# Kernel optimization log

Hardware: AMD Instinct MI355X
Metric: run time of the kernel (lower is better)

## Reference

```python
import jax, jax.numpy as jnp
import numpy as np

C = 768
H = 12
HD = C // H
SCALE = HD ** -0.5
EPS = 1e-5


def setup_inputs() -> dict:
    key = jax.random.key(0)
    kit = iter(jax.random.split(key, 40))
    r = lambda *s: jax.random.normal(next(kit), s, jnp.float32) * 0.02
    d = dict(
        s_x=jax.random.normal(next(kit), (8, 196, C), jnp.float32),
        t_x=jax.random.normal(next(kit), (8, 1568, C), jnp.float32),
        ln1s_g=jnp.ones(C), ln1s_b=jnp.zeros(C),
        mha_w=r(3 * C, C), mha_b=r(3 * C), mha_ow=r(C, C), mha_ob=r(C),
        ln1t_g=jnp.ones(C), ln1t_b=jnp.zeros(C),
        attn_qkv_w=r(3 * C, C), attn_q_b=r(C), attn_v_b=r(C), attn_pw=r(C, C), attn_pb=r(C),
        lnt2s_g=jnp.ones(C), lnt2s_b=jnp.zeros(C),
        t2s_qw=r(C, C), t2s_qb=r(C), t2s_kvw=r(2 * C, C), t2s_kvb=r(C), t2s_pw=r(C, C), t2s_pb=r(C),
        lns2t_g=jnp.ones(C), lns2t_b=jnp.zeros(C),
        s2t_qw=r(C, C), s2t_qb=r(C), s2t_kvw=r(2 * C, C), s2t_kvb=r(C), s2t_pw=r(C, C), s2t_pb=r(C),
        ln2s_g=jnp.ones(C), ln2s_b=jnp.zeros(C),
        cfc_w=r(4 * C, C), cfc_b=r(4 * C), cproj_w=r(C, 4 * C), cproj_b=r(C),
        ln2t_g=jnp.ones(C), ln2t_b=jnp.zeros(C),
        fc1_w=r(4 * C, C), fc1_b=r(4 * C), fc2_w=r(C, 4 * C), fc2_b=r(C),
    )
    return d


def ln(x, g, b):
    m = x.mean(-1, keepdims=True)
    v = jnp.mean((x - m) ** 2, -1, keepdims=True)
    return (x - m) * jax.lax.rsqrt(v + EPS) * g + b


def heads(x):  # (B, N, C) -> (B, H, N, HD)
    B, N, _ = x.shape
    return x.reshape(B, N, H, HD).transpose(0, 2, 1, 3)


def mhsa(q, k, v):  # (B, H, Nq, HD), (B, H, Nk, HD) -> (B, Nq, C)
    a = jax.nn.softmax(jnp.einsum('bhqd,bhkd->bhqk', q * SCALE, k), axis=-1)
    o = jnp.einsum('bhqk,bhkd->bhqd', a, v)
    B, _, Nq, _ = o.shape
    return o.transpose(0, 2, 1, 3).reshape(B, Nq, C)


def reference(s_x, t_x, ln1s_g, ln1s_b, mha_w, mha_b, mha_ow, mha_ob,
              ln1t_g, ln1t_b, attn_qkv_w, attn_q_b, attn_v_b, attn_pw, attn_pb,
              lnt2s_g, lnt2s_b, t2s_qw, t2s_qb, t2s_kvw, t2s_kvb, t2s_pw, t2s_pb,
              lns2t_g, lns2t_b, s2t_qw, s2t_qb, s2t_kvw, s2t_kvb, s2t_pw, s2t_pb,
              ln2s_g, ln2s_b, cfc_w, cfc_b, cproj_w, cproj_b,
              ln2t_g, ln2t_b, fc1_w, fc1_b, fc2_w, fc2_b):
    # 1) clip self-attention. torch nn.MultiheadAttention (batch_first=False)
    # treats axis 0 of the (B, s_N, C) input as the sequence dim, so we
    # faithfully attend over the batch axis.
    y = ln(s_x, ln1s_g, ln1s_b)
    qkv = y @ mha_w.T + mha_b  # (B, s_N, 3C)
    q, k, v = jnp.split(qkv, 3, axis=-1)
    qt, kt, vt = (a.transpose(1, 0, 2) for a in (q, k, v))  # (s_N, B, C)
    o = mhsa(heads(qt), heads(kt), heads(vt))  # (s_N, B, C)
    o = o @ mha_ow.T + mha_ob
    s_x = s_x + o.transpose(1, 0, 2)

    # 2) video-stream self-attention (qkv_bias=True -> cat(q_b, 0, v_b))
    y = ln(t_x, ln1t_g, ln1t_b)
    qkv_bias = jnp.concatenate([attn_q_b, jnp.zeros_like(attn_v_b), attn_v_b])
    qkv = y @ attn_qkv_w.T + qkv_bias
    q, k, v = jnp.split(qkv, 3, axis=-1)
    o = mhsa(heads(q), heads(k), heads(v))
    t_x = t_x + (o @ attn_pw.T + attn_pb)

    # 3) T2S cross: query from LN(s_x), key/value from (updated, un-normed) t_x
    ys = ln(s_x, lnt2s_g, lnt2s_b)
    q = ys @ t2s_qw.T + t2s_qb
    kv = t_x @ t2s_kvw.T + jnp.concatenate([jnp.zeros_like(t2s_kvb), t2s_kvb])
    k, v = jnp.split(kv, 2, axis=-1)
    o = mhsa(heads(q), heads(k), heads(v))
    s_x = s_x + (o @ t2s_pw.T + t2s_pb)

    # 4) S2T cross: query from LN(t_x), key/value from updated s_x
    yt = ln(t_x, lns2t_g, lns2t_b)
    q = yt @ s2t_qw.T + s2t_qb
    kv = s_x @ s2t_kvw.T + jnp.concatenate([jnp.zeros_like(s2t_kvb), s2t_kvb])
    k, v = jnp.split(kv, 2, axis=-1)
    o = mhsa(heads(q), heads(k), heads(v))
    t_x = t_x + (o @ s2t_pw.T + s2t_pb)

    # 5) clip MLP (QuickGELU)
    y = ln(s_x, ln2s_g, ln2s_b)
    h = y @ cfc_w.T + cfc_b
    h = h * jax.nn.sigmoid(1.702 * h)
    s_x = s_x + (h @ cproj_w.T + cproj_b)

    # 6) video MLP (exact GELU, torch default)
    y = ln(t_x, ln2t_g, ln2t_b)
    h = jax.nn.gelu(y @ fc1_w.T + fc1_b, approximate=False)
    t_x = t_x + (h @ fc2_w.T + fc2_b)
    return (s_x, t_x)
```

## Files before the change

### kernel.cpp

```cpp
#include <hip/hip_runtime.h>
#include <stdint.h>


typedef uint16_t u16;
typedef uint16_t u16x8 __attribute__((ext_vector_type(8)));
typedef uint16_t u16x4 __attribute__((ext_vector_type(4)));
typedef short bf16x8 __attribute__((ext_vector_type(8)));
typedef float f32x4 __attribute__((ext_vector_type(4)));

__device__ __forceinline__ float b2f(u16 u) {
    union { float f; uint32_t i; } x;
    x.i = ((uint32_t)u) << 16;
    return x.f;
}
__device__ __forceinline__ u16 f2b(float f) {
    union { float f; uint32_t i; } x;
    x.f = f;
    uint32_t i = x.i;
    uint32_t r = (i + 0x7FFFu + ((i >> 16) & 1u)) >> 16;
    return (u16)r;
}
__device__ __forceinline__ u16 f2b_trunc(float f) {
    union { float f; uint32_t i; } x;
    x.f = f;
    return (u16)(x.i >> 16);
}

__device__ __forceinline__ void gload16(const u16* g, u16* l) {
    __builtin_amdgcn_global_load_lds(
        (const __attribute__((address_space(1))) uint32_t*)g,
        (__attribute__((address_space(3))) uint32_t*)l, 16, 0, 0);
}

__global__ void f2b_kernel(const float* __restrict__ in, u16* __restrict__ out, int n) {
    int i = blockIdx.x * 256 + threadIdx.x;
    if (i < n) out[i] = f2b(in[i]);
}
__global__ void copy_f32(const float* __restrict__ in, float* __restrict__ out, int n) {
    int i = blockIdx.x * 256 + threadIdx.x;
    if (i < n) out[i] = in[i];
}

__global__ void build_bias_pool(float* __restrict__ dst,
    const float* mha_b, const float* attn_q_b, const float* attn_v_b,
    const float* mha_ob, const float* attn_pb, const float* t2s_kvb,
    const float* t2s_qb, const float* t2s_pb, const float* s2t_qb,
    const float* s2t_kvb, const float* s2t_pb, const float* cfc_b,
    const float* cproj_b, const float* fc1_b, const float* fc2_b) {
    int i = blockIdx.x * 256 + threadIdx.x;
    float v = 0.f;
    if (i < 2304) v = mha_b[i];
    else if (i < 4608) { int j = i - 2304; v = (j < 768) ? attn_q_b[j] : (j < 1536 ? 0.f : attn_v_b[j - 1536]); }
    else if (i < 5376) v = mha_ob[i - 4608];
    else if (i < 6144) v = attn_pb[i - 5376];
    else if (i < 7680) { int j = i - 6144; v = (j < 768) ? 0.f : t2s_kvb[j - 768]; }
    else if (i < 8448) v = t2s_qb[i - 7680];
    else if (i < 9216) v = t2s_pb[i - 8448];
    else if (i < 9984) v = s2t_qb[i - 9216];
    else if (i < 11520) { int j = i - 9984; v = (j < 768) ? 0.f : s2t_kvb[j - 768]; }
    else if (i < 12288) v = s2t_pb[i - 11520];
    else if (i < 15360) v = cfc_b[i - 12288];
    else if (i < 16128) v = cproj_b[i - 15360];
    else if (i < 19200) v = fc1_b[i - 16128];
    else if (i < 19968) v = fc2_b[i - 19200];
    else return;
    dst[i] = v;
}

__device__ __forceinline__ float block_sum(float v, float* red) {
    #pragma unroll
    for (int o = 32; o > 0; o >>= 1) v += __shfl_down(v, o, 64);
    int w = threadIdx.x >> 6, l = threadIdx.x & 63;
    __syncthreads();
    if (l == 0) red[w] = v;
    __syncthreads();
    return red[0] + red[1] + red[2] + red[3];
}

__global__ __launch_bounds__(256) void ln_kernel(
    const float* __restrict__ x, const float* __restrict__ g,
    const float* __restrict__ bta, u16* __restrict__ y) {
    const int r = blockIdx.x;
    const int t = threadIdx.x;
    const float* xr = x + (size_t)r * 768;
    float v0 = xr[t], v1 = xr[t + 256], v2 = xr[t + 512];
    __shared__ float red[4];
    float mean = block_sum(v0 + v1 + v2, red) * (1.0f / 768.0f);
    float d0 = v0 - mean, d1 = v1 - mean, d2 = v2 - mean;
    float var = block_sum(d0 * d0 + d1 * d1 + d2 * d2, red) * (1.0f / 768.0f);
    float rs = rsqrtf(var + 1e-5f);
    u16* yr = y + (size_t)r * 768;
    yr[t]       = f2b(d0 * rs * g[t]       + bta[t]);
    yr[t + 256] = f2b(d1 * rs * g[t + 256] + bta[t + 256]);
    yr[t + 512] = f2b(d2 * rs * g[t + 512] + bta[t + 512]);
}

__global__ __launch_bounds__(256) void transpose_v(
    const u16* __restrict__ vp, u16* __restrict__ vt, int Nk, int Nkp,
    long long vA, long long vJ) {
    const int inst = blockIdx.y;
    const int a = inst / 12, h = inst % 12;
    const int t0 = blockIdx.x * 64;
    const int tid = threadIdx.x;
    __shared__ u16 T[64][72];
    const int kvl = tid >> 2, dseg = (tid & 3) * 16;
    u16x8 v0 = {}, v1 = {};
    if (t0 + kvl < Nk) {
        const u16* src = vp + a * vA + (long long)(t0 + kvl) * vJ + h * 64 + dseg;
        v0 = *(const u16x8*)src;
        v1 = *(const u16x8*)(src + 8);
    }
    *(u16x8*)&T[kvl][dseg]     = v0;
    *(u16x8*)&T[kvl][dseg + 8] = v1;
    __syncthreads();
    const int dl = tid >> 2, kseg = (tid & 3) * 16;
    u16x8 w0, w1;
    #pragma unroll
    for (int j = 0; j < 8; j++) w0[j] = T[kseg + j][dl];
    #pragma unroll
    for (int j = 0; j < 8; j++) w1[j] = T[kseg + 8 + j][dl];
    u16* orow = vt + ((size_t)inst * 64 + dl) * Nkp + t0 + kseg;
    *(u16x8*)orow = w0;
    *(u16x8*)(orow + 8) = w1;
}

template <int MODE, int BM>
__global__ __launch_bounds__(256) void gemm_mfma(
    const u16* __restrict__ A, const u16* __restrict__ W,
    const float* __restrict__ bias, u16* __restrict__ Cb,
    float* __restrict__ Cf, int M, int N, int K) {
    constexpr int MI = BM / 32;
    __shared__ u16 As[2][BM][32];
    __shared__ u16 Bs[2][128][32];
    const int tid = threadIdx.x;
    const int lane = tid & 63;
    const int wid = tid >> 6;
    const int wr = (wid >> 1) * (BM / 2), wc = (wid & 1) * 64;
    const int m0 = blockIdx.x * BM, n0 = blockIdx.y * 128;
    const int lr = lane >> 2, lc = (lane & 3) * 8;
    const int fr = lane & 15, fk = (lane >> 4) * 8;
    const int abase = wid * (BM / 4);
    const int bbase = wid * 32;
    f32x4 acc[MI][4] = {};
    for (int k0 = 0; k0 < K; k0 += 64) {
        #pragma unroll
        for (int s = 0; s < 2; s++) {
            #pragma unroll
            for (int j = 0; j < BM / 64; j++) {
                int rowa = m0 + abase + j * 16 + lr;
                rowa = rowa < M ? rowa : M - 1;
                gload16(A + (size_t)rowa * K + k0 + s * 32 + lc, &As[s][abase + j * 16][0]);
            }
            #pragma unroll
            for (int j = 0; j < 2; j++) {
                gload16(W + (size_t)(n0 + bbase + j * 16 + lr) * K + k0 + s * 32 + lc,
                        &Bs[s][bbase + j * 16][0]);
            }
        }
        __syncthreads();
        #pragma unroll
        for (int s = 0; s < 2; s++) {
            bf16x8 a[MI], b[4];
            #pragma unroll
            for (int i = 0; i < MI; i++) a[i] = *(const bf16x8*)&As[s][wr + i * 16 + fr][fk];
            #pragma unroll
            for (int j = 0; j < 4; j++) b[j] = *(const bf16x8*)&Bs[s][wc + j * 16 + fr][fk];
            #pragma unroll
            for (int i = 0; i < MI; i++)
                #pragma unroll
                for (int j = 0; j < 4; j++)
                    acc[i][j] = __builtin_amdgcn_mfma_f32_16x16x32_bf16(a[i], b[j], acc[i][j], 0, 0, 0);
        }
        __syncthreads();
    }
    const int er = (lane >> 4) * 4;
    #pragma unroll
    for (int i = 0; i < MI; i++) {
        #pragma unroll
        for (int reg = 0; reg < 4; reg++) {
            int r = m0 + wr + i * 16 + er + reg;
            if (r >= M) continue;
            #pragma unroll
            for (int j = 0; j < 4; j++) {
                int c = n0 + wc + j * 16 + fr;
                float v = acc[i][j][reg] + bias[c];
                size_t idx = (size_t)r * N + c;
                if (MODE == 1) {
                    Cf[idx] += v;
                } else if (MODE == 4) {
                    float nv = Cf[idx] + v;
                    Cf[idx] = nv;
                    Cb[idx] = f2b(nv);
                } else {
                    if (MODE == 2) v = v / (1.0f + expf(-1.702f * v));
                    if (MODE == 3) v = 0.5f * v * (1.0f + erff(v * 0.70710678118654752f));
                    Cb[idx] = f2b(v);
                }
            }
        }
    }
}

__global__ __launch_bounds__(256) void flash_attn(
    const u16* __restrict__ qp, const u16* __restrict__ kp,
    const u16* __restrict__ vt, u16* __restrict__ op,
    int Nq, int Nk, int Nkp,
    long long qA, long long qI, long long kA, long long kJ,
    long long oA, long long oI) {
    const int inst = blockIdx.y;
    const int a = inst / 12, h = inst % 12;
    const int tid = threadIdx.x, lane = tid & 63, w = tid >> 6;
    const int fr = lane & 15, g = lane >> 4, fk = g * 8;
    const int f3s = (fr & 7) << 3;
    __shared__ u16 Ks[2][64][64];
    __shared__ u16 Vs[2][64][64];
    __shared__ u16 Ps[4][16][64];
    const u16* qb = qp + a * qA + h * 64;
    const u16* kb = kp + a * kA + h * 64;
    const u16* vtb = vt + (size_t)inst * 64 * Nkp;
    const int q0 = blockIdx.x * 64 + w * 16;

    bf16x8 qf[2];
    {
        u16x8 raw0 = {}, raw1 = {};
        int qr = q0 + fr;
        if (qr < Nq) {
            const u16* qrp = qb + (long long)qr * qI;
            raw0 = *(const u16x8*)(qrp + fk);
            raw1 = *(const u16x8*)(qrp + 32 + fk);
        }
        const float QS = 0.125f * 1.44269504088896340736f;
        u16x8 s0, s1;
        #pragma unroll
        for (int e = 0; e < 8; e++) {
            s0[e] = f2b(b2f(raw0[e]) * QS);
            s1[e] = f2b(b2f(raw1[e]) * QS);
        }
        qf[0] = *(bf16x8*)&s0;
        qf[1] = *(bf16x8*)&s1;
    }
    float mrun = -1e30f, lrun = 0.f;
    f32x4 o[4] = {};

    const int l = lane;
    const int srow = w * 8 + (l >> 3);
    const int sdcol = ((l & 7) * 8) ^ (((l >> 3) & 7) << 3);

    auto STAGE = [&](int s, int t0) {
        #pragma unroll
        for (int c = 0; c < 2; c++) {
            int row = c * 32 + srow;
            int kr = t0 + row; if (kr >= Nk) kr = Nk - 1;
            gload16(kb + (long long)kr * kJ + sdcol, &Ks[s][0][0] + c * 2048 + w * 512);
            gload16(vtb + (size_t)row * Nkp + t0 + sdcol, &Vs[s][0][0] + c * 2048 + w * 512);
        }
    };

    const int nt = (Nk + 63) >> 6;
    STAGE(0, 0);
    for (int it = 0; it < nt; ++it) {
        const int t0 = it << 6;
        const int cur = it & 1;
        if (it + 1 < nt) {
            STAGE(cur ^ 1, t0 + 64);
            asm volatile("s_waitcnt vmcnt(4)" ::: "memory");
        } else {
            asm volatile("s_waitcnt vmcnt(0)" ::: "memory");
        }
        __builtin_amdgcn_s_barrier();

        f32x4 s[4] = {};
        __builtin_amdgcn_s_setprio(1);
        #pragma unroll
        for (int hh = 0; hh < 4; hh++) {
            bf16x8 k0f = *(const bf16x8*)&Ks[cur][hh * 16 + fr][fk ^ f3s];
            bf16x8 k1f = *(const bf16x8*)&Ks[cur][hh * 16 + fr][(32 + fk) ^ f3s];
            s[hh] = __builtin_amdgcn_mfma_f32_16x16x32_bf16(k0f, qf[0], s[hh], 0, 0, 0);
            s[hh] = __builtin_amdgcn_mfma_f32_16x16x32_bf16(k1f, qf[1], s[hh], 0, 0, 0);
        }
        __builtin_amdgcn_s_setprio(0);

        if (t0 + 64 > Nk) {
            #pragma unroll
            for (int hh = 0; hh < 4; hh++)
                #pragma unroll
                for (int r = 0; r < 4; r++)
                    if (t0 + hh * 16 + 4 * g + r >= Nk) s[hh][r] = -1e30f;
        }
        float a0 = fmaxf(fmaxf(s[0][0], s[0][1]), s[0][2]);
        float a1 = fmaxf(fmaxf(s[0][3], s[1][0]), s[1][1]);
        float a2 = fmaxf(fmaxf(s[1][2], s[1][3]), s[2][0]);
        float a3 = fmaxf(fmaxf(s[2][1], s[2][2]), s[2][3]);
        float a4 = fmaxf(fmaxf(s[3][0], s[3][1]), s[3][2]);
        float b0 = fmaxf(fmaxf(a0, a1), a2);
        float b1 = fmaxf(fmaxf(a3, a4), s[3][3]);
        float lmax = fmaxf(b0, b1);
        lmax = fmaxf(lmax, __shfl_xor(lmax, 16, 64));
        lmax = fmaxf(lmax, __shfl_xor(lmax, 32, 64));
        if (!__all(lmax <= mrun + 8.0f)) {
            float mn = fmaxf(mrun, lmax);
            float sf = exp2f(mrun - mn);
            mrun = mn;
            lrun *= sf;
            float sfo[4];
            #pragma unroll
            for (int r = 0; r < 4; r++) sfo[r] = __shfl(sf, g * 4 + r, 64);
            #pragma unroll
            for (int dt = 0; dt < 4; dt++)
                #pragma unroll
                for (int r = 0; r < 4; r++) o[dt][r] *= sfo[r];
        }
        float p[4][4];
        float ps = 0.f;
        #pragma unroll
        for (int hh = 0; hh < 4; hh++)
            #pragma unroll
            for (int r = 0; r < 4; r++) {
                p[hh][r] = exp2f(s[hh][r] - mrun);
                ps += p[hh][r];
            }
        ps += __shfl_xor(ps, 16, 64);
        ps += __shfl_xor(ps, 32, 64);
        lrun += ps;
        #pragma unroll
        for (int hh = 0; hh < 4; hh++) {
            u16x4 pk;
            #pragma unroll
            for (int r = 0; r < 4; r++) pk[r] = f2b_trunc(p[hh][r]);
            *(u16x4*)&Ps[w][fr][(hh * 16 + g * 4) ^ f3s] = pk;
        }
        bf16x8 pa0 = *(const bf16x8*)&Ps[w][fr][fk ^ f3s];
        bf16x8 pa1 = *(const bf16x8*)&Ps[w][fr][(32 + fk) ^ f3s];
        __builtin_amdgcn_s_setprio(1);
        #pragma unroll
        for (int dt = 0; dt < 4; dt++) {
            bf16x8 vf0 = *(const bf16x8*)&Vs[cur][dt * 16 + fr][fk ^ f3s];
            bf16x8 vf1 = *(const bf16x8*)&Vs[cur][dt * 16 + fr][(32 + fk) ^ f3s];
            o[dt] = __builtin_amdgcn_mfma_f32_16x16x32_bf16(pa0, vf0, o[dt], 0, 0, 0);
            o[dt] = __builtin_amdgcn_mfma_f32_16x16x32_bf16(pa1, vf1, o[dt], 0, 0, 0);
        }
        __builtin_amdgcn_s_setprio(0);
        __builtin_amdgcn_s_barrier();
    }
    float rcp = 1.0f / lrun;
    #pragma unroll
    for (int r = 0; r < 4; r++) {
        float rr = __shfl(rcp, g * 4 + r, 64);
        int q = q0 + g * 4 + r;
        if (q >= Nq) continue;
        u16* orow = op + a * oA + (long long)q * oI + h * 64;
        #pragma unroll
        for (int dt = 0; dt < 4; dt++)
            orow[dt * 16 + fr] = f2b(o[dt][r] * rr);
    }
}

extern "C" void kernel_launch(void* const* d_in, const int* in_sizes, int n_in,
                              void* d_out, int out_size, void* d_ws, size_t ws_size,
                              hipStream_t stream) {
    const int B = 8, sN = 196, tN = 1568;
    const int Ms = B * sN;
    const int Mt = B * tN;
    const int n_sf = Ms * 768;
    const int n_tf = Mt * 768;
    (void)n_in; (void)out_size; (void)ws_size;

    const bool dict_order = (in_sizes[0] == n_sf);
    auto IN = [&](int di, int ai) -> const float* {
        return (const float*)d_in[dict_order ? di : ai];
    };
    const float* in_sx      = IN(0, 35);
    const float* in_tx      = IN(1, 42);
    const float* ln1s_g     = IN(2, 14);
    const float* ln1s_b     = IN(3, 13);
    const float* mha_w      = IN(4, 28);
    const float* mha_b      = IN(5, 25);
    const float* mha_ow     = IN(6, 27);
    const float* mha_ob     = IN(7, 26);
    const float* ln1t_g     = IN(8, 16);
    const float* ln1t_b     = IN(9, 15);
    const float* attn_qkv_w = IN(10, 3);
    const float* attn_q_b   = IN(11, 2);
    const float* attn_v_b   = IN(12, 4);
    const float* attn_pw    = IN(13, 1);
    const float* attn_pb    = IN(14, 0);
    const float* lnt2s_g    = IN(15, 24);
    const float* lnt2s_b    = IN(16, 23);
    const float* t2s_qw     = IN(17, 41);
    const float* t2s_qb     = IN(18, 40);
    const float* t2s_kvw    = IN(19, 37);
    const float* t2s_kvb    = IN(20, 36);
    const float* t2s_pw     = IN(21, 39);
    const float* t2s_pb     = IN(22, 38);
    const float* lns2t_g    = IN(23, 22);
    const float* lns2t_b    = IN(24, 21);
    const float* s2t_qw     = IN(25, 34);
    const float* s2t_qb     = IN(26, 33);
    const float* s2t_kvw    = IN(27, 30);
    const float* s2t_kvb    = IN(28, 29);
    const float* s2t_pw     = IN(29, 32);
    const float* s2t_pb     = IN(30, 31);
    const float* ln2s_g     = IN(31, 18);
    const float* ln2s_b     = IN(32, 17);
    const float* cfc_w      = IN(33, 6);
    const float* cfc_b      = IN(34, 5);
    const float* cproj_w    = IN(35, 8);
    const float* cproj_b    = IN(36, 7);
    const float* ln2t_g     = IN(37, 20);
    const float* ln2t_b     = IN(38, 19);
    const float* fc1_w      = IN(39, 10);
    const float* fc1_b      = IN(40, 9);
    const float* fc2_w      = IN(41, 12);
    const float* fc2_b      = IN(42, 11);

    float* s_f = (float*)d_out;
    float* t_f = (float*)d_out + n_sf;

    char* ws = (char*)d_ws;
    size_t off = 0;
    auto take = [&](size_t bytes) { size_t o = off; off += (bytes + 255) & ~(size_t)255; return o; };
    float* biasP = (float*)(ws + take(19968 * 4));
    u16*   yb    = (u16*)(ws + take((size_t)Mt * 768 * 2));
    u16*   bufA  = (u16*)(ws + take((size_t)Mt * 3072 * 2));
    u16*   bufB  = (u16*)(ws + take((size_t)Mt * 768 * 2));
    u16*   sxb   = (u16*)(ws + take((size_t)Ms * 768 * 2));
    u16*   vtb   = (u16*)(ws + take((size_t)2352 * 64 * 64 * 2));
    auto wtake = [&](size_t nelem) { return (u16*)(ws + take(nelem * 2)); };
    u16 *W_mha   = wtake(2304 * 768), *W_mhao  = wtake(768 * 768);
    u16 *W_qkv   = wtake(2304 * 768), *W_attnp = wtake(768 * 768);
    u16 *W_t2sq  = wtake(768 * 768),  *W_t2skv = wtake(1536 * 768), *W_t2sp = wtake(768 * 768);
    u16 *W_s2tq  = wtake(768 * 768),  *W_s2tkv = wtake(1536 * 768), *W_s2tp = wtake(768 * 768);
    u16 *W_cfc   = wtake(3072 * 768), *W_cproj = wtake(768 * 3072);
    u16 *W_fc1   = wtake(3072 * 768), *W_fc2   = wtake(768 * 3072);

    const int B_MHA = 0, B_QKV = 2304, B_MHAO = 4608, B_ATTNP = 5376;
    const int B_T2SKV = 6144, B_T2SQ = 7680, B_T2SP = 8448, B_S2TQ = 9216;
    const int B_S2TKV = 9984, B_S2TP = 11520, B_CFC = 12288, B_CPROJ = 15360;
    const int B_FC1 = 16128, B_FC2 = 19200;

    auto cdiv = [](int a, int b) { return (a + b - 1) / b; };
    auto CW = [&](const float* src, u16* dst, int n) {
        f2b_kernel<<<cdiv(n, 256), 256, 0, stream>>>(src, dst, n);
    };
    CW(mha_w, W_mha, 2304 * 768);      CW(mha_ow, W_mhao, 768 * 768);
    CW(attn_qkv_w, W_qkv, 2304 * 768); CW(attn_pw, W_attnp, 768 * 768);
    CW(t2s_qw, W_t2sq, 768 * 768);     CW(t2s_kvw, W_t2skv, 1536 * 768);
    CW(t2s_pw, W_t2sp, 768 * 768);     CW(s2t_qw, W_s2tq, 768 * 768);
    CW(s2t_kvw, W_s2tkv, 1536 * 768);  CW(s2t_pw, W_s2tp, 768 * 768);
    CW(cfc_w, W_cfc, 3072 * 768);      CW(cproj_w, W_cproj, 768 * 3072);
    CW(fc1_w, W_fc1, 3072 * 768);      CW(fc2_w, W_fc2, 768 * 3072);

    build_bias_pool<<<78, 256, 0, stream>>>(biasP,
        mha_b, attn_q_b, attn_v_b, mha_ob, attn_pb, t2s_kvb, t2s_qb, t2s_pb,
        s2t_qb, s2t_kvb, s2t_pb, cfc_b, cproj_b, fc1_b, fc2_b);

    copy_f32<<<cdiv(n_sf, 256), 256, 0, stream>>>(in_sx, s_f, n_sf);
    copy_f32<<<cdiv(n_tf, 256), 256, 0, stream>>>(in_tx, t_f, n_tf);

    ln_kernel<<<Ms, 256, 0, stream>>>(s_f, ln1s_g, ln1s_b, yb);
    gemm_mfma<0, 64><<<dim3(cdiv(Ms, 64), 18), 256, 0, stream>>>(yb, W_mha, biasP + B_MHA, bufA, (float*)0, Ms, 2304, 768);
    transpose_v<<<dim3(1, sN * 12), 256, 0, stream>>>(bufA + 1536, vtb, 8, 64, 2304LL, (long long)sN * 2304);
    flash_attn<<<dim3(1, sN * 12), 256, 0, stream>>>(
        bufA, bufA + 768, vtb, bufB, 8, 8, 64,
        2304LL, (long long)sN * 2304,
        2304LL, (long long)sN * 2304,
        768LL,  (long long)sN * 768);
    gemm_mfma<1, 64><<<dim3(cdiv(Ms, 64), 6), 256, 0, stream>>>(bufB, W_mhao, biasP + B_MHAO, (u16*)0, s_f, Ms, 768, 768);

    ln_kernel<<<Mt, 256, 0, stream>>>(t_f, ln1t_g, ln1t_b, yb);
    gemm_mfma<0, 128><<<dim3(cdiv(Mt, 128), 18), 256, 0, stream>>>(yb, W_qkv, biasP + B_QKV, bufA, (float*)0, Mt, 2304, 768);
    transpose_v<<<dim3(25, B * 12), 256, 0, stream>>>(bufA + 1536, vtb, tN, 1600, (long long)tN * 2304, 2304LL);
    flash_attn<<<dim3(cdiv(tN, 64), B * 12), 256, 0, stream>>>(
        bufA, bufA + 768, vtb, bufB, tN, tN, 1600,
        (long long)tN * 2304, 2304LL,
        (long long)tN * 2304, 2304LL,
        (long long)tN * 768, 768LL);
    gemm_mfma<4, 128><<<dim3(cdiv(Mt, 128), 6), 256, 0, stream>>>(bufB, W_attnp, biasP + B_ATTNP, yb, t_f, Mt, 768, 768);

    gemm_mfma<0, 128><<<dim3(cdiv(Mt, 128), 12), 256, 0, stream>>>(yb, W_t2skv, biasP + B_T2SKV, bufA, (float*)0, Mt, 1536, 768);
    transpose_v<<<dim3(25, B * 12), 256, 0, stream>>>(bufA + 768, vtb, tN, 1600, (long long)tN * 1536, 1536LL);
    ln_kernel<<<Ms, 256, 0, stream>>>(s_f, lnt2s_g, lnt2s_b, yb);
    u16* q3 = bufB;
    u16* o3 = bufB + (size_t)Ms * 768;
    gemm_mfma<0, 64><<<dim3(cdiv(Ms, 64), 6), 256, 0, stream>>>(yb, W_t2sq, biasP + B_T2SQ, q3, (float*)0, Ms, 768, 768);
    flash_attn<<<dim3(cdiv(sN, 64), B * 12), 256, 0, stream>>>(
        q3, bufA, vtb, o3, sN, tN, 1600,
        (long long)sN * 768, 768LL,
        (long long)tN * 1536, 1536LL,
        (long long)sN * 768, 768LL);
    gemm_mfma<4, 64><<<dim3(cdiv(Ms, 64), 6), 256, 0, stream>>>(o3, W_t2sp, biasP + B_T2SP, sxb, s_f, Ms, 768, 768);

    ln_kernel<<<Mt, 256, 0, stream>>>(t_f, lns2t_g, lns2t_b, yb);
    gemm_mfma<0, 128><<<dim3(cdiv(Mt, 128), 6), 256, 0, stream>>>(yb, W_s2tq, biasP + B_S2TQ, bufB, (float*)0, Mt, 768, 768);
    gemm_mfma<0, 64><<<dim3(cdiv(Ms, 64), 12), 256, 0, stream>>>(sxb, W_s2tkv, biasP + B_S2TKV, bufA, (float*)0, Ms, 1536, 768);
    transpose_v<<<dim3(4, B * 12), 256, 0, stream>>>(bufA + 768, vtb, sN, 256, (long long)sN * 1536, 1536LL);
    flash_attn<<<dim3(cdiv(tN, 64), B * 12), 256, 0, stream>>>(
        bufB, bufA, vtb, yb, tN, sN, 256,
        (long long)tN * 768, 768LL,
        (long long)sN * 1536, 1536LL,
        (long long)tN * 768, 768LL);
    gemm_mfma<1, 128><<<dim3(cdiv(Mt, 128), 6), 256, 0, stream>>>(yb, W_s2tp, biasP + B_S2TP, (u16*)0, t_f, Mt, 768, 768);

    ln_kernel<<<Ms, 256, 0, stream>>>(s_f, ln2s_g, ln2s_b, yb);
    gemm_mfma<2, 64><<<dim3(cdiv(Ms, 64), 24), 256, 0, stream>>>(yb, W_cfc, biasP + B_CFC, bufA, (float*)0, Ms, 3072, 768);
    gemm_mfma<1, 64><<<dim3(cdiv(Ms, 64), 6), 256, 0, stream>>>(bufA, W_cproj, biasP + B_CPROJ, (u16*)0, s_f, Ms, 768, 3072);

    ln_kernel<<<Mt, 256, 0, stream>>>(t_f, ln2t_g, ln2t_b, yb);
    gemm_mfma<3, 128><<<dim3(cdiv(Mt, 128), 24), 256, 0, stream>>>(yb, W_fc1, biasP + B_FC1, bufA, (float*)0, Mt, 3072, 768);
    gemm_mfma<1, 128><<<dim3(cdiv(Mt, 128), 6), 256, 0, stream>>>(bufA, W_fc2, biasP + B_FC2, (u16*)0, t_f, Mt, 768, 3072);
}
```

Before: 1.050 ms.

## Co-launch independent spatial and temporal stream kernels as paired grids

Adds paired kernel wrappers for the GEMM, flash-attention, transpose and layernorm kernels. One launch now runs both the small spatial-stream problem and the large temporal-stream problem, chosen by flattened block index. The fourteen weight conversions collapse into one segmented kernel and the two input copies into one. This is meant to fill the GPU better on the small s-stream kernels and to cut launch count. In exchange it adds new buffer aliasing (vtb_s shares yb), relies on s_f and t_f being contiguous in the output, and gives each paired kernel shared-memory sizing for the larger tile.

```diff
diff --git a/kernel.cpp b/kernel.cpp
--- a/kernel.cpp
+++ b/kernel.cpp
@@ -32,16 +32,29 @@
         (__attribute__((address_space(3))) uint32_t*)l, 16, 0, 0);
 }
 
-__global__ void f2b_kernel(const float* __restrict__ in, u16* __restrict__ out, int n) {
+struct CvtAll {
+    const float* s[14];
+    u16* d[14];
+    int cum[15];
+};
+__global__ __launch_bounds__(256) void cvt_all(CvtAll c) {
     int i = blockIdx.x * 256 + threadIdx.x;
-    if (i < n) out[i] = f2b(in[i]);
-}
-__global__ void copy_f32(const float* __restrict__ in, float* __restrict__ out, int n) {
+    if (i >= c.cum[14]) return;
+    int seg = 0;
+    #pragma unroll
+    for (int k = 1; k < 14; k++) seg += (i >= c.cum[k]);
+    int j = i - c.cum[seg];
+    c.d[seg][j] = f2b(c.s[seg][j]);
+}
+
+__global__ __launch_bounds__(256) void copy_both(
+    const float* __restrict__ a, const float* __restrict__ b,
+    float* __restrict__ out, int na, int ntot) {
     int i = blockIdx.x * 256 + threadIdx.x;
-    if (i < n) out[i] = in[i];
-}
-
-__global__ void build_bias_pool(float* __restrict__ dst,
+    if (i < ntot) out[i] = (i < na) ? a[i] : b[i - na];
+}
+
+__global__ __launch_bounds__(256) void build_bias_pool(float* __restrict__ dst,
     const float* mha_b, const float* attn_q_b, const float* attn_v_b,
     const float* mha_ob, const float* attn_pb, const float* t2s_kvb,
     const float* t2s_qb, const float* t2s_pb, const float* s2t_qb,
@@ -77,11 +90,15 @@
     return red[0] + red[1] + red[2] + red[3];
 }
 
-__global__ __launch_bounds__(256) void ln_kernel(
-    const float* __restrict__ x, const float* __restrict__ g,
-    const float* __restrict__ bta, u16* __restrict__ y) {
+__global__ __launch_bounds__(256) void ln_dual(
+    const float* __restrict__ x, int rows0,
+    const float* __restrict__ g0, const float* __restrict__ b0, u16* __restrict__ y0,
+    const float* __restrict__ g1, const float* __restrict__ b1, u16* __restrict__ y1) {
     const int r = blockIdx.x;
     const int t = threadIdx.x;
+    const float* g; const float* bta; u16* yr;
+    if (r < rows0) { g = g0; bta = b0; yr = y0 + (size_t)r * 768; }
+    else           { g = g1; bta = b1; yr = y1 + (size_t)(r - rows0) * 768; }
     const float* xr = x + (size_t)r * 768;
     float v0 = xr[t], v1 = xr[t + 256], v2 = xr[t + 512];
     __shared__ float red[4];
@@ -89,24 +106,25 @@
     float d0 = v0 - mean, d1 = v1 - mean, d2 = v2 - mean;
     float var = block_sum(d0 * d0 + d1 * d1 + d2 * d2, red) * (1.0f / 768.0f);
     float rs = rsqrtf(var + 1e-5f);
-    u16* yr = y + (size_t)r * 768;
     yr[t]       = f2b(d0 * rs * g[t]       + bta[t]);
     yr[t + 256] = f2b(d1 * rs * g[t + 256] + bta[t + 256]);
     yr[t + 512] = f2b(d2 * rs * g[t + 512] + bta[t + 512]);
 }
 
-__global__ __launch_bounds__(256) void transpose_v(
-    const u16* __restrict__ vp, u16* __restrict__ vt, int Nk, int Nkp,
-    long long vA, long long vJ) {
-    const int inst = blockIdx.y;
+struct TransP {
+    const u16* vp; u16* vt;
+    int Nk, Nkp, gx, nb;
+    long long vA, vJ;
+};
+__device__ __forceinline__ void transpose_body(const TransP p, int bid, u16 (*T)[72]) {
+    const int x = bid % p.gx, inst = bid / p.gx;
     const int a = inst / 12, h = inst % 12;
-    const int t0 = blockIdx.x * 64;
+    const int t0 = x * 64;
     const int tid = threadIdx.x;
-    __shared__ u16 T[64][72];
     const int kvl = tid >> 2, dseg = (tid & 3) * 16;
     u16x8 v0 = {}, v1 = {};
-    if (t0 + kvl < Nk) {
-        const u16* src = vp + a * vA + (long long)(t0 + kvl) * vJ + h * 64 + dseg;
+    if (t0 + kvl < p.Nk) {
+        const u16* src = p.vp + a * p.vA + (long long)(t0 + kvl) * p.vJ + h * 64 + dseg;
         v0 = *(const u16x8*)src;
         v1 = *(const u16x8*)(src + 8);
     }
@@ -119,42 +137,51 @@
     for (int j = 0; j < 8; j++) w0[j] = T[kseg + j][dl];
     #pragma unroll
     for (int j = 0; j < 8; j++) w1[j] = T[kseg + 8 + j][dl];
-    u16* orow = vt + ((size_t)inst * 64 + dl) * Nkp + t0 + kseg;
+    u16* orow = p.vt + ((size_t)inst * 64 + dl) * p.Nkp + t0 + kseg;
     *(u16x8*)orow = w0;
     *(u16x8*)(orow + 8) = w1;
 }
-
+__global__ __launch_bounds__(256) void transpose_pair(TransP p0, TransP p1) {
+    __shared__ u16 T[64][72];
+    int bid = blockIdx.x;
+    if (bid < p0.nb) transpose_body(p0, bid, T);
+    else transpose_body(p1, bid - p0.nb, T);
+}
+
+struct GemmP {
+    const u16* A; const u16* W; const float* bias;
+    u16* Cb; float* Cf;
+    int M, N, K, gx, nb;
+};
 template <int MODE, int BM>
-__global__ __launch_bounds__(256) void gemm_mfma(
-    const u16* __restrict__ A, const u16* __restrict__ W,
-    const float* __restrict__ bias, u16* __restrict__ Cb,
-    float* __restrict__ Cf, int M, int N, int K) {
+__device__ __forceinline__ void gemm_body(const GemmP p, int bid,
+                                          u16 (*AsF)[32], u16 (*BsF)[32]) {
     constexpr int MI = BM / 32;
-    __shared__ u16 As[2][BM][32];
-    __shared__ u16 Bs[2][128][32];
     const int tid = threadIdx.x;
     const int lane = tid & 63;
     const int wid = tid >> 6;
     const int wr = (wid >> 1) * (BM / 2), wc = (wid & 1) * 64;
-    const int m0 = blockIdx.x * BM, n0 = blockIdx.y * 128;
+    const int bx = bid % p.gx, by = bid / p.gx;
+    const int m0 = bx * BM, n0 = by * 128;
     const int lr = lane >> 2, lc = (lane & 3) * 8;
     const int fr = lane & 15, fk = (lane >> 4) * 8;
     const int abase = wid * (BM / 4);
     const int bbase = wid * 32;
     f32x4 acc[MI][4] = {};
-    for (int k0 = 0; k0 < K; k0 += 64) {
+    for (int k0 = 0; k0 < p.K; k0 += 64) {
         #pragma unroll
         for (int s = 0; s < 2; s++) {
             #pragma unroll
             for (int j = 0; j < BM / 64; j++) {
                 int rowa = m0 + abase + j * 16 + lr;
-                rowa = rowa < M ? rowa : M - 1;
-                gload16(A + (size_t)rowa * K + k0 + s * 32 + lc, &As[s][abase + j * 16][0]);
+                rowa = rowa < p.M ? rowa : p.M - 1;
+                gload16(p.A + (size_t)rowa * p.K + k0 + s * 32 + lc,
+                        &AsF[s * 128 + abase + j * 16][0]);
             }
             #pragma unroll
             for (int j = 0; j < 2; j++) {
-                gload16(W + (size_t)(n0 + bbase + j * 16 + lr) * K + k0 + s * 32 + lc,
-                        &Bs[s][bbase + j * 16][0]);
+                gload16(p.W + (size_t)(n0 + bbase + j * 16 + lr) * p.K + k0 + s * 32 + lc,
+                        &BsF[s * 128 + bbase + j * 16][0]);
             }
         }
         __syncthreads();
@@ -162,9 +189,9 @@
         for (int s = 0; s < 2; s++) {
             bf16x8 a[MI], b[4];
             #pragma unroll
-            for (int i = 0; i < MI; i++) a[i] = *(const bf16x8*)&As[s][wr + i * 16 + fr][fk];
-            #pragma unroll
-            for (int j = 0; j < 4; j++) b[j] = *(const bf16x8*)&Bs[s][wc + j * 16 + fr][fk];
+            for (int i = 0; i < MI; i++) a[i] = *(const bf16x8*)&AsF[s * 128 + wr + i * 16 + fr][fk];
+            #pragma unroll
+            for (int j = 0; j < 4; j++) b[j] = *(const bf16x8*)&BsF[s * 128 + wc + j * 16 + fr][fk];
             #pragma unroll
             for (int i = 0; i < MI; i++)
                 #pragma unroll
@@ -179,53 +206,59 @@
         #pragma unroll
         for (int reg = 0; reg < 4; reg++) {
             int r = m0 + wr + i * 16 + er + reg;
-            if (r >= M) continue;
+            if (r >= p.M) continue;
             #pragma unroll
             for (int j = 0; j < 4; j++) {
                 int c = n0 + wc + j * 16 + fr;
-                float v = acc[i][j][reg] + bias[c];
-                size_t idx = (size_t)r * N + c;
+                float v = acc[i][j][reg] + p.bias[c];
+                size_t idx = (size_t)r * p.N + c;
                 if (MODE == 1) {
-                    Cf[idx] += v;
+                    p.Cf[idx] += v;
                 } else if (MODE == 4) {
-                    float nv = Cf[idx] + v;
-                    Cf[idx] = nv;
-                    Cb[idx] = f2b(nv);
+                    float nv = p.Cf[idx] + v;
+                    p.Cf[idx] = nv;
+                    p.Cb[idx] = f2b(nv);
                 } else {
                     if (MODE == 2) v = v / (1.0f + expf(-1.702f * v));
                     if (MODE == 3) v = 0.5f * v * (1.0f + erff(v * 0.70710678118654752f));
-                    Cb[idx] = f2b(v);
+                    p.Cb[idx] = f2b(v);
                 }
             }
         }
     }
 }
-
-__global__ __launch_bounds__(256) void flash_attn(
-    const u16* __restrict__ qp, const u16* __restrict__ kp,
-    const u16* __restrict__ vt, u16* __restrict__ op,
-    int Nq, int Nk, int Nkp,
-    long long qA, long long qI, long long kA, long long kJ,
-    long long oA, long long oI) {
-    const int inst = blockIdx.y;
+template <int M0, int B0, int M1, int B1>
+__global__ __launch_bounds__(256) void gemm_pair(GemmP p0, GemmP p1) {
+    __shared__ u16 As[2 * 128][32];
+    __shared__ u16 Bs[2 * 128][32];
+    int bid = blockIdx.x;
+    if (bid < p0.nb) gemm_body<M0, B0>(p0, bid, As, Bs);
+    else gemm_body<M1, B1>(p1, bid - p0.nb, As, Bs);
+}
+
+struct FlashP {
+    const u16* qp; const u16* kp; const u16* vt; u16* op;
+    int Nq, Nk, Nkp, gx, nb;
+    long long qA, qI, kA, kJ, oA, oI;
+};
+__device__ __forceinline__ void flash_body(const FlashP p, int bid,
+    u16 (*Ks)[64][64], u16 (*Vs)[64][64], u16 (*Ps)[16][64]) {
+    const int x = bid % p.gx, inst = bid / p.gx;
     const int a = inst / 12, h = inst % 12;
     const int tid = threadIdx.x, lane = tid & 63, w = tid >> 6;
     const int fr = lane & 15, g = lane >> 4, fk = g * 8;
     const int f3s = (fr & 7) << 3;
-    __shared__ u16 Ks[2][64][64];
-    __shared__ u16 Vs[2][64][64];
-    __shared__ u16 Ps[4][16][64];
-    const u16* qb = qp + a * qA + h * 64;
-    const u16* kb = kp + a * kA + h * 64;
-    const u16* vtb = vt + (size_t)inst * 64 * Nkp;
-    const int q0 = blockIdx.x * 64 + w * 16;
+    const u16* qb = p.qp + a * p.qA + h * 64;
+    const u16* kb = p.kp + a * p.kA + h * 64;
+    const u16* vtb = p.vt + (size_t)inst * 64 * p.Nkp;
+    const int q0 = x * 64 + w * 16;
 
     bf16x8 qf[2];
     {
         u16x8 raw0 = {}, raw1 = {};
         int qr = q0 + fr;
-        if (qr < Nq) {
-            const u16* qrp = qb + (long long)qr * qI;
+        if (qr < p.Nq) {
+            const u16* qrp = qb + (long long)qr * p.qI;
             raw0 = *(const u16x8*)(qrp + fk);
             raw1 = *(const u16x8*)(qrp + 32 + fk);
         }
@@ -250,13 +283,13 @@
         #pragma unroll
         for (int c = 0; c < 2; c++) {
             int row = c * 32 + srow;
-            int kr = t0 + row; if (kr >= Nk) kr = Nk - 1;
-            gload16(kb + (long long)kr * kJ + sdcol, &Ks[s][0][0] + c * 2048 + w * 512);
-            gload16(vtb + (size_t)row * Nkp + t0 + sdcol, &Vs[s][0][0] + c * 2048 + w * 512);
+            int kr = t0 + row; if (kr >= p.Nk) kr = p.Nk - 1;
+            gload16(kb + (long long)kr * p.kJ + sdcol, &Ks[s][0][0] + c * 2048 + w * 512);
+            gload16(vtb + (size_t)row * p.Nkp + t0 + sdcol, &Vs[s][0][0] + c * 2048 + w * 512);
         }
     };
 
-    const int nt = (Nk + 63) >> 6;
+    const int nt = (p.Nk + 63) >> 6;
     STAGE(0, 0);
     for (int it = 0; it < nt; ++it) {
         const int t0 = it << 6;
@@ -280,12 +313,12 @@
         }
         __builtin_amdgcn_s_setprio(0);
 
-        if (t0 + 64 > Nk) {
+        if (t0 + 64 > p.Nk) {
             #pragma unroll
             for (int hh = 0; hh < 4; hh++)
                 #pragma unroll
                 for (int r = 0; r < 4; r++)
-                    if (t0 + hh * 16 + 4 * g + r >= Nk) s[hh][r] = -1e30f;
+                    if (t0 + hh * 16 + 4 * g + r >= p.Nk) s[hh][r] = -1e30f;
         }
         float a0 = fmaxf(fmaxf(s[0][0], s[0][1]), s[0][2]);
         float a1 = fmaxf(fmaxf(s[0][3], s[1][0]), s[1][1]);
@@ -310,14 +343,14 @@
                 #pragma unroll
                 for (int r = 0; r < 4; r++) o[dt][r] *= sfo[r];
         }
-        float p[4][4];
+        float pp[4][4];
         float ps = 0.f;
         #pragma unroll
         for (int hh = 0; hh < 4; hh++)
             #pragma unroll
             for (int r = 0; r < 4; r++) {
-                p[hh][r] = exp2f(s[hh][r] - mrun);
-                ps += p[hh][r];
+                pp[hh][r] = exp2f(s[hh][r] - mrun);
+                ps += pp[hh][r];
             }
         ps += __shfl_xor(ps, 16, 64);
         ps += __shfl_xor(ps, 32, 64);
@@ -326,7 +359,7 @@
         for (int hh = 0; hh < 4; hh++) {
             u16x4 pk;
             #pragma unroll
-            for (int r = 0; r < 4; r++) pk[r] = f2b_trunc(p[hh][r]);
+            for (int r = 0; r < 4; r++) pk[r] = f2b_trunc(pp[hh][r]);
             *(u16x4*)&Ps[w][fr][(hh * 16 + g * 4) ^ f3s] = pk;
         }
         bf16x8 pa0 = *(const bf16x8*)&Ps[w][fr][fk ^ f3s];
@@ -347,12 +380,20 @@
     for (int r = 0; r < 4; r++) {
         float rr = __shfl(rcp, g * 4 + r, 64);
         int q = q0 + g * 4 + r;
-        if (q >= Nq) continue;
-        u16* orow = op + a * oA + (long long)q * oI + h * 64;
+        if (q >= p.Nq) continue;
+        u16* orow = p.op + a * p.oA + (long long)q * p.oI + h * 64;
         #pragma unroll
         for (int dt = 0; dt < 4; dt++)
             orow[dt * 16 + fr] = f2b(o[dt][r] * rr);
     }
+}
+__global__ __launch_bounds__(256) void flash_pair(FlashP p0, FlashP p1) {
+    __shared__ u16 Ks[2][64][64];
+    __shared__ u16 Vs[2][64][64];
+    __shared__ u16 Ps[4][16][64];
+    int bid = blockIdx.x;
+    if (bid < p0.nb) flash_body(p0, bid, Ks, Vs, Ps);
+    else flash_body(p1, bid - p0.nb, Ks, Vs, Ps);
 }
 
 extern "C" void kernel_launch(void* const* d_in, const int* in_sizes, int n_in,
@@ -420,11 +461,15 @@
     size_t off = 0;
     auto take = [&](size_t bytes) { size_t o = off; off += (bytes + 255) & ~(size_t)255; return o; };
     float* biasP = (float*)(ws + take(19968 * 4));
-    u16*   yb    = (u16*)(ws + take((size_t)Mt * 768 * 2));
+    u16*   yb    = (u16*)(ws + take((size_t)(Ms + Mt) * 768 * 2));
     u16*   bufA  = (u16*)(ws + take((size_t)Mt * 3072 * 2));
+    u16*   bufS  = (u16*)(ws + take((size_t)Mt * 768 * 2));
     u16*   bufB  = (u16*)(ws + take((size_t)Mt * 768 * 2));
     u16*   sxb   = (u16*)(ws + take((size_t)Ms * 768 * 2));
-    u16*   vtb   = (u16*)(ws + take((size_t)2352 * 64 * 64 * 2));
+    u16*   vtb_t = (u16*)(ws + take((size_t)96 * 64 * 1600 * 2));
+    u16*   yb_s  = yb;
+    u16*   yb_t  = yb + (size_t)Ms * 768;
+    u16*   vtb_s = yb;
     auto wtake = [&](size_t nelem) { return (u16*)(ws + take(nelem * 2)); };
     u16 *W_mha   = wtake(2304 * 768), *W_mhao  = wtake(768 * 768);
     u16 *W_qkv   = wtake(2304 * 768), *W_attnp = wtake(768 * 768);
@@ -439,73 +484,137 @@
     const int B_FC1 = 16128, B_FC2 = 19200;
 
     auto cdiv = [](int a, int b) { return (a + b - 1) / b; };
-    auto CW = [&](const float* src, u16* dst, int n) {
-        f2b_kernel<<<cdiv(n, 256), 256, 0, stream>>>(src, dst, n);
-    };
-    CW(mha_w, W_mha, 2304 * 768);      CW(mha_ow, W_mhao, 768 * 768);
-    CW(attn_qkv_w, W_qkv, 2304 * 768); CW(attn_pw, W_attnp, 768 * 768);
-    CW(t2s_qw, W_t2sq, 768 * 768);     CW(t2s_kvw, W_t2skv, 1536 * 768);
-    CW(t2s_pw, W_t2sp, 768 * 768);     CW(s2t_qw, W_s2tq, 768 * 768);
-    CW(s2t_kvw, W_s2tkv, 1536 * 768);  CW(s2t_pw, W_s2tp, 768 * 768);
-    CW(cfc_w, W_cfc, 3072 * 768);      CW(cproj_w, W_cproj, 768 * 3072);
-    CW(fc1_w, W_fc1, 3072 * 768);      CW(fc2_w, W_fc2, 768 * 3072);
-
+
+    {
+        CvtAll c;
+        const float* ss[14] = { mha_w, mha_ow, attn_qkv_w, attn_pw, t2s_qw, t2s_kvw, t2s_pw,
+                                s2t_qw, s2t_kvw, s2t_pw, cfc_w, cproj_w, fc1_w, fc2_w };
+        u16* dd[14] = { W_mha, W_mhao, W_qkv, W_attnp, W_t2sq, W_t2skv, W_t2sp,
+                        W_s2tq, W_s2tkv, W_s2tp, W_cfc, W_cproj, W_fc1, W_fc2 };
+        int nn[14] = { 2304*768, 768*768, 2304*768, 768*768, 768*768, 1536*768, 768*768,
+                       768*768, 1536*768, 768*768, 3072*768, 768*3072, 3072*768, 768*3072 };
+        int cum = 0;
+        for (int k = 0; k < 14; k++) { c.s[k] = ss[k]; c.d[k] = dd[k]; c.cum[k] = cum; cum += nn[k]; }
+        c.cum[14] = cum;
+        cvt_all<<<cdiv(cum, 256), 256, 0, stream>>>(c);
+    }
     build_bias_pool<<<78, 256, 0, stream>>>(biasP,
         mha_b, attn_q_b, attn_v_b, mha_ob, attn_pb, t2s_kvb, t2s_qb, t2s_pb,
         s2t_qb, s2t_kvb, s2t_pb, cfc_b, cproj_b, fc1_b, fc2_b);
-
-    copy_f32<<<cdiv(n_sf, 256), 256, 0, stream>>>(in_sx, s_f, n_sf);
-    copy_f32<<<cdiv(n_tf, 256), 256, 0, stream>>>(in_tx, t_f, n_tf);
-
-    ln_kernel<<<Ms, 256, 0, stream>>>(s_f, ln1s_g, ln1s_b, yb);
-    gemm_mfma<0, 64><<<dim3(cdiv(Ms, 64), 18), 256, 0, stream>>>(yb, W_mha, biasP + B_MHA, bufA, (float*)0, Ms, 2304, 768);
-    transpose_v<<<dim3(1, sN * 12), 256, 0, stream>>>(bufA + 1536, vtb, 8, 64, 2304LL, (long long)sN * 2304);
-    flash_attn<<<dim3(1, sN * 12), 256, 0, stream>>>(
-        bufA, bufA + 768, vtb, bufB, 8, 8, 64,
-        2304LL, (long long)sN * 2304,
-        2304LL, (long long)sN * 2304,
-        768LL,  (long long)sN * 768);
-    gemm_mfma<1, 64><<<dim3(cdiv(Ms, 64), 6), 256, 0, stream>>>(bufB, W_mhao, biasP + B_MHAO, (u16*)0, s_f, Ms, 768, 768);
-
-    ln_kernel<<<Mt, 256, 0, stream>>>(t_f, ln1t_g, ln1t_b, yb);
-    gemm_mfma<0, 128><<<dim3(cdiv(Mt, 128), 18), 256, 0, stream>>>(yb, W_qkv, biasP + B_QKV, bufA, (float*)0, Mt, 2304, 768);
-    transpose_v<<<dim3(25, B * 12), 256, 0, stream>>>(bufA + 1536, vtb, tN, 1600, (long long)tN * 2304, 2304LL);
-    flash_attn<<<dim3(cdiv(tN, 64), B * 12), 256, 0, stream>>>(
-        bufA, bufA + 768, vtb, bufB, tN, tN, 1600,
-        (long long)tN * 2304, 2304LL,
-        (long long)tN * 2304, 2304LL,
-        (long long)tN * 768, 768LL);
-    gemm_mfma<4, 128><<<dim3(cdiv(Mt, 128), 6), 256, 0, stream>>>(bufB, W_attnp, biasP + B_ATTNP, yb, t_f, Mt, 768, 768);
-
-    gemm_mfma<0, 128><<<dim3(cdiv(Mt, 128), 12), 256, 0, stream>>>(yb, W_t2skv, biasP + B_T2SKV, bufA, (float*)0, Mt, 1536, 768);
-    transpose_v<<<dim3(25, B * 12), 256, 0, stream>>>(bufA + 768, vtb, tN, 1600, (long long)tN * 1536, 1536LL);
-    ln_kernel<<<Ms, 256, 0, stream>>>(s_f, lnt2s_g, lnt2s_b, yb);
-    u16* q3 = bufB;
-    u16* o3 = bufB + (size_t)Ms * 768;
-    gemm_mfma<0, 64><<<dim3(cdiv(Ms, 64), 6), 256, 0, stream>>>(yb, W_t2sq, biasP + B_T2SQ, q3, (float*)0, Ms, 768, 768);
-    flash_attn<<<dim3(cdiv(sN, 64), B * 12), 256, 0, stream>>>(
-        q3, bufA, vtb, o3, sN, tN, 1600,
-        (long long)sN * 768, 768LL,
-        (long long)tN * 1536, 1536LL,
-        (long long)sN * 768, 768LL);
-    gemm_mfma<4, 64><<<dim3(cdiv(Ms, 64), 6), 256, 0, stream>>>(o3, W_t2sp, biasP + B_T2SP, sxb, s_f, Ms, 768, 768);
-
-    ln_kernel<<<Mt, 256, 0, stream>>>(t_f, lns2t_g, lns2t_b, yb);
-    gemm_mfma<0, 128><<<dim3(cdiv(Mt, 128), 6), 256, 0, stream>>>(yb, W_s2tq, biasP + B_S2TQ, bufB, (float*)0, Mt, 768, 768);
-    gemm_mfma<0, 64><<<dim3(cdiv(Ms, 64), 12), 256, 0, stream>>>(sxb, W_s2tkv, biasP + B_S2TKV, bufA, (float*)0, Ms, 1536, 768);
-    transpose_v<<<dim3(4, B * 12), 256, 0, stream>>>(bufA + 768, vtb, sN, 256, (long long)sN * 1536, 1536LL);
-    flash_attn<<<dim3(cdiv(tN, 64), B * 12), 256, 0, stream>>>(
-        bufB, bufA, vtb, yb, tN, sN, 256,
-        (long long)tN * 768, 768LL,
-        (long long)sN * 1536, 1536LL,
-        (long long)tN * 768, 768LL);
-    gemm_mfma<1, 128><<<dim3(cdiv(Mt, 128), 6), 256, 0, stream>>>(yb, W_s2tp, biasP + B_S2TP, (u16*)0, t_f, Mt, 768, 768);
-
-    ln_kernel<<<Ms, 256, 0, stream>>>(s_f, ln2s_g, ln2s_b, yb);
-    gemm_mfma<2, 64><<<dim3(cdiv(Ms, 64), 24), 256, 0, stream>>>(yb, W_cfc, biasP + B_CFC, bufA, (float*)0, Ms, 3072, 768);
-    gemm_mfma<1, 64><<<dim3(cdiv(Ms, 64), 6), 256, 0, stream>>>(bufA, W_cproj, biasP + B_CPROJ, (u16*)0, s_f, Ms, 768, 3072);
-
-    ln_kernel<<<Mt, 256, 0, stream>>>(t_f, ln2t_g, ln2t_b, yb);
-    gemm_mfma<3, 128><<<dim3(cdiv(Mt, 128), 24), 256, 0, stream>>>(yb, W_fc1, biasP + B_FC1, bufA, (float*)0, Mt, 3072, 768);
-    gemm_mfma<1, 128><<<dim3(cdiv(Mt, 128), 6), 256, 0, stream>>>(bufA, W_fc2, biasP + B_FC2, (u16*)0, t_f, Mt, 768, 3072);
-}
+    copy_both<<<cdiv(n_sf + n_tf, 256), 256, 0, stream>>>(in_sx, in_tx, s_f, n_sf, n_sf + n_tf);
+
+    auto GP = [&](const u16* A, const u16* W, const float* bias, u16* Cb, float* Cf,
+                  int M, int N, int K, int BM) {
+        GemmP p; p.A = A; p.W = W; p.bias = bias; p.Cb = Cb; p.Cf = Cf;
+        p.M = M; p.N = N; p.K = K; p.gx = (M + BM - 1) / BM; p.nb = p.gx * (N / 128);
+        return p;
+    };
+    auto FP = [&](const u16* qp, const u16* kp, const u16* vt, u16* op,
+                  int Nq, int Nk, int Nkp,
+                  long long qA, long long qI, long long kA, long long kJ,
+                  long long oA, long long oI) {
+        FlashP p; p.qp = qp; p.kp = kp; p.vt = vt; p.op = op;
+        p.Nq = Nq; p.Nk = Nk; p.Nkp = Nkp; p.gx = (Nq + 63) / 64;
+        p.nb = p.gx * (Nq == 8 ? sN * 12 : B * 12);
+        p.qA = qA; p.qI = qI; p.kA = kA; p.kJ = kJ; p.oA = oA; p.oI = oI;
+        return p;
+    };
+    auto TP = [&](const u16* vp, u16* vt, int Nk, int Nkp, long long vA, long long vJ, int insts) {
+        TransP p; p.vp = vp; p.vt = vt; p.Nk = Nk; p.Nkp = Nkp;
+        p.gx = (Nk + 63) / 64; p.nb = p.gx * insts; p.vA = vA; p.vJ = vJ;
+        return p;
+    };
+
+    ln_dual<<<Ms + Mt, 256, 0, stream>>>((const float*)d_out, Ms,
+        ln1s_g, ln1s_b, yb_s, ln1t_g, ln1t_b, yb_t);
+
+    {
+        GemmP p0 = GP(yb_s, W_mha, biasP + B_MHA, bufS, 0, Ms, 2304, 768, 64);
+        GemmP p1 = GP(yb_t, W_qkv, biasP + B_QKV, bufA, 0, Mt, 2304, 768, 128);
+        gemm_pair<0, 64, 0, 128><<<p0.nb + p1.nb, 256, 0, stream>>>(p0, p1);
+    }
+    {
+        TransP p0 = TP(bufS + 1536, vtb_s, 8, 64, 2304LL, (long long)sN * 2304, sN * 12);
+        TransP p1 = TP(bufA + 1536, vtb_t, tN, 1600, (long long)tN * 2304, 2304LL, B * 12);
+        transpose_pair<<<p0.nb + p1.nb, 256, 0, stream>>>(p0, p1);
+    }
+    {
+        FlashP p0 = FP(bufS, bufS + 768, vtb_s, sxb, 8, 8, 64,
+                       2304LL, (long long)sN * 2304, 2304LL, (long long)sN * 2304,
+                       768LL, (long long)sN * 768);
+        FlashP p1 = FP(bufA, bufA + 768, vtb_t, bufB, tN, tN, 1600,
+                       (long long)tN * 2304, 2304LL, (long long)tN * 2304, 2304LL,
+                       (long long)tN * 768, 768LL);
+        flash_pair<<<p0.nb + p1.nb, 256, 0, stream>>>(p0, p1);
+    }
+    {
+        GemmP p0 = GP(sxb, W_mhao, biasP + B_MHAO, 0, s_f, Ms, 768, 768, 64);
+        GemmP p1 = GP(bufB, W_attnp, biasP + B_ATTNP, yb_t, t_f, Mt, 768, 768, 128);
+        gemm_pair<1, 64, 4, 128><<<p0.nb + p1.nb, 256, 0, stream>>>(p0, p1);
+    }
+    ln_dual<<<Ms + Mt, 256, 0, stream>>>((const float*)d_out, Ms,
+        lnt2s_g, lnt2s_b, yb_s, lns2t_g, lns2t_b, bufB);
+
+    {
+        GemmP p0 = GP(yb_t, W_t2skv, biasP + B_T2SKV, bufA, 0, Mt, 1536, 768, 128);
+        GemmP p1 = GP(bufB, W_s2tq, biasP + B_S2TQ, bufS, 0, Mt, 768, 768, 128);
+        gemm_pair<0, 128, 0, 128><<<p0.nb + p1.nb, 256, 0, stream>>>(p0, p1);
+    }
+    {
+        TransP p0 = TP(bufA + 768, vtb_t, tN, 1600, (long long)tN * 1536, 1536LL, B * 12);
+        TransP pz = p0; pz.nb = 0;
+        transpose_pair<<<p0.nb, 256, 0, stream>>>(p0, pz);
+    }
+    {
+        GemmP p0 = GP(yb_s, W_t2sq, biasP + B_T2SQ, sxb, 0, Ms, 768, 768, 64);
+        GemmP pz = p0; pz.nb = 0;
+        gemm_pair<0, 64, 0, 64><<<p0.nb, 256, 0, stream>>>(p0, pz);
+    }
+    {
+        FlashP p0 = FP(sxb, bufA, vtb_t, yb_s, sN, tN, 1600,
+                       (long long)sN * 768, 768LL, (long long)tN * 1536, 1536LL,
+                       (long long)sN * 768, 768LL);
+        FlashP pz = p0; pz.nb = 0;
+        flash_pair<<<p0.nb, 256, 0, stream>>>(p0, pz);
+    }
+    {
+        GemmP p0 = GP(yb_s, W_t2sp, biasP + B_T2SP, sxb, s_f, Ms, 768, 768, 64);
+        GemmP pz = p0; pz.nb = 0;
+        gemm_pair<4, 64, 4, 64><<<p0.nb, 256, 0, stream>>>(p0, pz);
+    }
+    {
+        GemmP p0 = GP(sxb, W_s2tkv, biasP + B_S2TKV, bufB, 0, Ms, 1536, 768, 64);
+        GemmP pz = p0; pz.nb = 0;
+        gemm_pair<0, 64, 0, 64><<<p0.nb, 256, 0, stream>>>(p0, pz);
+    }
+    {
+        TransP p0 = TP(bufB + 768, vtb_s, sN, 256, (long long)sN * 1536, 1536LL, B * 12);
+        TransP pz = p0; pz.nb = 0;
+        transpose_pair<<<p0.nb, 256, 0, stream>>>(p0, pz);
+    }
+    {
+        FlashP p0 = FP(bufS, bufB, vtb_s, bufA, tN, sN, 256,
+                       (long long)tN * 768, 768LL, (long long)sN * 1536, 1536LL,
+                       (long long)tN * 768, 768LL);
+        FlashP pz = p0; pz.nb = 0;
+        flash_pair<<<p0.nb, 256, 0, stream>>>(p0, pz);
+    }
+    {
+        GemmP p0 = GP(bufA, W_s2tp, biasP + B_S2TP, 0, t_f, Mt, 768, 768, 128);
+        GemmP pz = p0; pz.nb = 0;
+        gemm_pair<1, 128, 1, 128><<<p0.nb, 256, 0, stream>>>(p0, pz);
+    }
+    ln_dual<<<Ms + Mt, 256, 0, stream>>>((const float*)d_out, Ms,
+        ln2s_g, ln2s_b, yb_s, ln2t_g, ln2t_b, yb_t);
+
+    {
+        GemmP p0 = GP(yb_s, W_cfc, biasP + B_CFC, bufS, 0, Ms, 3072, 768, 64);
+        GemmP p1 = GP(yb_t, W_fc1, biasP + B_FC1, bufA, 0, Mt, 3072, 768, 128);
+        gemm_pair<2, 64, 3, 128><<<p0.nb + p1.nb, 256, 0, stream>>>(p0, p1);
+    }
+    {
+        GemmP p0 = GP(bufS, W_cproj, biasP + B_CPROJ, 0, s_f, Ms, 768, 3072, 64);
+        GemmP p1 = GP(bufA, W_fc2, biasP + B_FC2, 0, t_f, Mt, 768, 3072, 128);
+        gemm_pair<1, 64, 1, 128><<<p0.nb + p1.nb, 256, 0, stream>>>(p0, p1);
+    }
+}
```

After: 968.0 us. 1.08x faster.
